# Kernel optimization log

Hardware: AMD Instinct MI355X
Metric: run time of the kernel (lower is better)

## Reference

```python
import jax, jax.numpy as jnp
import numpy as np

T, E, H, V, K = 1024, 300, 512, 100000, 12
START, STOP = 10, 11


def setup_inputs() -> dict:
    key = jax.random.key(0)
    ks = jax.random.split(key, 12)
    s = 0.05
    sentence = jax.random.randint(ks[0], (T,), 0, V, dtype=jnp.int32)
    tags = jax.random.randint(ks[1], (T,), 0, START, dtype=jnp.int32)  # real tags only
    word_embeds = jax.random.normal(ks[2], (V, E), jnp.float32) * 0.1

    def lstm_p(k):
        k1, k2 = jax.random.split(k)
        return (jax.random.normal(k1, (4 * H, E), jnp.float32) * s,
                jax.random.normal(k2, (4 * H, H), jnp.float32) * s,
                jnp.zeros(4 * H, jnp.float32), jnp.zeros(4 * H, jnp.float32))

    Wih_f, Whh_f, bih_f, bhh_f = lstm_p(ks[3])
    Wih_b, Whh_b, bih_b, bhh_b = lstm_p(ks[4])
    D = 2 * H
    attn_W = jax.random.normal(ks[5], (D, D), jnp.float32) * s
    attn_b = jnp.zeros(D, jnp.float32)
    h2h1_W = jax.random.normal(ks[6], (D, 2 * D), jnp.float32) * s
    h2h1_b = jnp.zeros(D, jnp.float32)
    tag_W = jax.random.normal(ks[7], (K, D), jnp.float32) * s
    tag_b = jnp.zeros(K, jnp.float32)
    transitions = jax.random.normal(ks[8], (K, K), jnp.float32) * 0.01
    transitions = transitions.at[START, :].set(-10000.0).at[:, STOP].set(-10000.0)
    return dict(sentence=sentence, tags=tags, word_embeds=word_embeds,
                Wih_f=Wih_f, Whh_f=Whh_f, bih_f=bih_f, bhh_f=bhh_f,
                Wih_b=Wih_b, Whh_b=Whh_b, bih_b=bih_b, bhh_b=bhh_b,
                attn_W=attn_W, attn_b=attn_b, h2h1_W=h2h1_W, h2h1_b=h2h1_b,
                tag_W=tag_W, tag_b=tag_b, transitions=transitions)


def _lstm_pass(x, Wih, Whh, bih, bhh):
    # x: [T, E] -> hs: [T, H]   (PyTorch LSTM gate order i,f,g,o)
    xg = x @ Wih.T + bih  # [T, 4H] precomputed input contribution

    def step(carry, g_in):
        h, c = carry
        g = g_in + h @ Whh.T + bhh
        i, f, gg, o = jnp.split(g, 4)
        i = jax.nn.sigmoid(i); f = jax.nn.sigmoid(f)
        gg = jnp.tanh(gg); o = jax.nn.sigmoid(o)
        c = f * c + i * gg
        h = o * jnp.tanh(c)
        return (h, c), h

    init = (jnp.zeros(H, x.dtype), jnp.zeros(H, x.dtype))
    _, hs = jax.lax.scan(step, init, xg)
    return hs


def reference(sentence, tags, word_embeds, Wih_f, Whh_f, bih_f, bhh_f,
              Wih_b, Whh_b, bih_b, bhh_b, attn_W, attn_b,
              h2h1_W, h2h1_b, tag_W, tag_b, transitions):
    x = word_embeds[sentence]                       # [T, E]  (dropout is eval no-op)
    h_fwd = _lstm_pass(x, Wih_f, Whh_f, bih_f, bhh_f)
    h_bwd = _lstm_pass(x[::-1], Wih_b, Whh_b, bih_b, bhh_b)[::-1]
    enc = jnp.concatenate([h_fwd, h_bwd], axis=-1)  # [T, 2H]

    # Attn 'general': energy(t, i) = enc[t] . (W enc[i] + b); vectorized per-timestep loop
    proj = enc @ attn_W.T + attn_b                  # [T, 2H]
    scores = enc @ proj.T                           # [T, T]
    w = jax.nn.softmax(scores, axis=-1)
    ctx = w @ enc                                   # [T, 2H]

    h1 = jnp.tanh(jnp.concatenate([enc, ctx], axis=-1) @ h2h1_W.T + h2h1_b)  # [T, 2H]
    feats = h1 @ tag_W.T + tag_b                    # [T, K]

    # CRF forward algorithm (log partition); transitions[to, from]
    alpha0 = jnp.full((K,), -10000.0, feats.dtype).at[START].set(0.0)

    def crf_step(alpha, feat):
        a = jax.nn.logsumexp(alpha[None, :] + transitions, axis=1) + feat
        return a, None

    alpha, _ = jax.lax.scan(crf_step, alpha0, feats)
    logZ = jax.nn.logsumexp(alpha + transitions[STOP])

    # gold path score (_score_sentence)
    pad_start = jnp.concatenate([jnp.array([START], tags.dtype), tags])
    pad_stop = jnp.concatenate([tags, jnp.array([STOP], tags.dtype)])
    gold = transitions[pad_stop, pad_start].sum() + feats[jnp.arange(T), tags].sum()

    return logZ - gold  # CRF negative log-likelihood for this sentence
```

## Files before the change

kernel.cpp:

```cpp
#include <hip/hip_runtime.h>
#include <hip/hip_fp16.h>

#define T_LEN 1024
#define E_DIM 300
#define H_DIM 512
#define D_DIM 1024
#define K_TAGS 12
#define G4 2048

typedef __attribute__((ext_vector_type(8))) short short8x;
typedef __attribute__((ext_vector_type(4))) float f32x4;

static __device__ __forceinline__ float frcp(float x){ return __builtin_amdgcn_rcpf(x); }
static __device__ __forceinline__ float sigm(float x){ return frcp(1.f + __expf(-x)); }
static __device__ __forceinline__ float ftanh(float x){
  const float e = __expf(2.f * fabsf(x));
  const float t = 1.f - 2.f * frcp(e + 1.f);
  return copysignf(t, x);
}
static __device__ __forceinline__ unsigned short f2b(float f){
  unsigned u = __float_as_uint(f);
  return (unsigned short)((u + 0x7fffu + ((u >> 16) & 1u)) >> 16);
}
static __device__ __forceinline__ uint4 pack8(const float* s){
  uint4 o;
  o.x = (unsigned)f2b(s[0]) | ((unsigned)f2b(s[1]) << 16);
  o.y = (unsigned)f2b(s[2]) | ((unsigned)f2b(s[3]) << 16);
  o.z = (unsigned)f2b(s[4]) | ((unsigned)f2b(s[5]) << 16);
  o.w = (unsigned)f2b(s[6]) | ((unsigned)f2b(s[7]) << 16);
  return o;
}

__global__ void k_gather(const int* __restrict__ sent, const float* __restrict__ we,
                         float* __restrict__ x){
  int idx = blockIdx.x*256 + threadIdx.x;
  if (idx < T_LEN*E_DIM){
    int t = idx / E_DIM, e = idx - t*E_DIM;
    x[idx] = we[(size_t)sent[t]*E_DIM + e];
  }
}

__global__ void k_init(unsigned* __restrict__ hbuf){
  int i = blockIdx.x*256 + threadIdx.x;
  if (i < 2048) hbuf[i] = 0u;
}

__global__ __launch_bounds__(256) void k_gemm_mfma(
    const float* __restrict__ Af, int lda, int arev,
    const float* __restrict__ Bf, const unsigned short* __restrict__ Bh, int ldb,
    const float* __restrict__ bias, int act,
    float* __restrict__ C, int ldc, int M, int N, int K)
{
  __shared__ __align__(16) unsigned short As[64*40];
  __shared__ __align__(16) unsigned short Bs[64*40];
  const int tid = threadIdx.x;
  const int bm = blockIdx.y*64, bn = blockIdx.x*64;
  const int r  = tid >> 2, c8 = (tid & 3) * 8;
  const int wave = tid >> 6, lane = tid & 63;
  const int wm = (wave >> 1) * 32, wn = (wave & 1) * 32;
  const int col = lane & 15, quad = lane >> 4;

  const int am = arev ? (M-1-(bm+r)) : (bm+r);
  const float* arow = Af + (size_t)am*lda;
  const float* brow = Bf ? (Bf + (size_t)(bn+r)*ldb) : (const float*)0;
  const unsigned short* brh = Bh ? (Bh + (size_t)(bn+r)*ldb) : (const unsigned short*)0;

  uint4* aw = (uint4*)(As + r*40 + c8);
  uint4* bw = (uint4*)(Bs + r*40 + c8);

  f32x4 acc[2][2];
  #pragma unroll
  for (int i=0;i<2;i++)
    #pragma unroll
    for (int j=0;j<2;j++) acc[i][j] = (f32x4){0.f,0.f,0.f,0.f};

  for (int k0 = 0; k0 < K; k0 += 32){
    uint4 avv, bvv;
    if (k0 + 32 <= K){
      avv = pack8(arow + k0 + c8);
      bvv = Bh ? *(const uint4*)(brh + k0 + c8) : pack8(brow + k0 + c8);
    } else {
      float ta[8], tb[8];
      #pragma unroll
      for (int i=0;i<8;i++){
        const int kk = k0 + c8 + i;
        ta[i] = (kk < K) ? arow[kk] : 0.f;
        tb[i] = (kk < K && Bf) ? brow[kk] : 0.f;
      }
      avv = pack8(ta); bvv = pack8(tb);
    }
    if (k0) __syncthreads();
    *aw = avv; *bw = bvv;
    __syncthreads();
    const short8x a0 = *(const short8x*)(As + (wm+col)*40    + quad*8);
    const short8x a1 = *(const short8x*)(As + (wm+16+col)*40 + quad*8);
    const short8x b0 = *(const short8x*)(Bs + (wn+col)*40    + quad*8);
    const short8x b1 = *(const short8x*)(Bs + (wn+16+col)*40 + quad*8);
    acc[0][0] = __builtin_amdgcn_mfma_f32_16x16x32_bf16(a0, b0, acc[0][0], 0, 0, 0);
    acc[0][1] = __builtin_amdgcn_mfma_f32_16x16x32_bf16(a0, b1, acc[0][1], 0, 0, 0);
    acc[1][0] = __builtin_amdgcn_mfma_f32_16x16x32_bf16(a1, b0, acc[1][0], 0, 0, 0);
    acc[1][1] = __builtin_amdgcn_mfma_f32_16x16x32_bf16(a1, b1, acc[1][1], 0, 0, 0);
  }

  #pragma unroll
  for (int mt=0;mt<2;mt++){
    #pragma unroll
    for (int nt=0;nt<2;nt++){
      const int cc = bn + wn + 16*nt + col;
      const float bs = bias ? bias[cc] : 0.f;
      #pragma unroll
      for (int i=0;i<4;i++){
        const int rr = bm + wm + 16*mt + quad*4 + i;
        float v = acc[mt][nt][i] + bs;
        if (act) v = ftanh(v);
        C[(size_t)rr*ldc + cc] = v;
      }
    }
  }
}

__global__ __launch_bounds__(256, 1) void k_lstm(
    const float* __restrict__ Whh_f, const float* __restrict__ Whh_b,
    const float* __restrict__ bih_f, const float* __restrict__ bhh_f,
    const float* __restrict__ bih_b, const float* __restrict__ bhh_b,
    const float* __restrict__ xg_f, const float* __restrict__ xg_b,
    unsigned* __restrict__ hbuf, float* __restrict__ enc)
{
  const int dir = blockIdx.x >> 5;
  const int w   = blockIdx.x & 31;
  const int tid = threadIdx.x;
  const int wave = tid >> 6, lane = tid & 63;
  const int col = lane & 15, quad = lane >> 4;

  const float* Whh = dir ? Whh_b : Whh_f;
  const float* xg  = dir ? xg_b  : xg_f;

  const int rowA = wave*H_DIM + w*16 + col;
  short8x w_frag[16];
  #pragma unroll
  for (int s=0;s<16;s++){
    const float* bp = Whh + (size_t)rowA*H_DIM + s*32 + quad*8;
    uint4 u = pack8(bp);
    w_frag[s] = *reinterpret_cast<short8x*>(&u);
  }

  float bias_r = 0.f, xg_cur = 0.f, c_reg = 0.f;
  int row2 = 0;
  if (tid < 64){
    row2 = (tid >> 4)*H_DIM + w*16 + (tid & 15);
    bias_r = dir ? (bih_b[row2] + bhh_b[row2]) : (bih_f[row2] + bhh_f[row2]);
    xg_cur = xg[row2];
  }

  __shared__ __align__(16) unsigned short lds_hb[512];
  __shared__ __align__(16) float raw[64];

  unsigned* hb = hbuf + dir*1024;

  for (int t = 1; t <= T_LEN; ++t){
    {
      unsigned* s0 = hb + ((t-1)&1)*512 + tid;
      const unsigned want = (unsigned)(t-1);
      unsigned v0 = __hip_atomic_load(s0,     __ATOMIC_RELAXED, __HIP_MEMORY_SCOPE_AGENT);
      unsigned v1 = __hip_atomic_load(s0+256, __ATOMIC_RELAXED, __HIP_MEMORY_SCOPE_AGENT);
      while (((v0 >> 16) != want) || ((v1 >> 16) != want)){
        v0 = __hip_atomic_load(s0,     __ATOMIC_RELAXED, __HIP_MEMORY_SCOPE_AGENT);
        v1 = __hip_atomic_load(s0+256, __ATOMIC_RELAXED, __HIP_MEMORY_SCOPE_AGENT);
      }
      lds_hb[tid]     = f2b(__half2float(__ushort_as_half((unsigned short)(v0 & 0xffffu))));
      lds_hb[tid+256] = f2b(__half2float(__ushort_as_half((unsigned short)(v1 & 0xffffu))));
    }
    __syncthreads();

    float xg_nxt = 0.f;
    if (tid < 64 && t < T_LEN) xg_nxt = xg[(size_t)t*G4 + row2];

    f32x4 a0 = (f32x4){0.f,0.f,0.f,0.f}, a1 = (f32x4){0.f,0.f,0.f,0.f};
    #pragma unroll
    for (int s=0;s<16;s+=2){
      const short8x b0 = *(const short8x*)(lds_hb + s*32     + quad*8);
      const short8x b1 = *(const short8x*)(lds_hb + (s+1)*32 + quad*8);
      a0 = __builtin_amdgcn_mfma_f32_16x16x32_bf16(w_frag[s],   b0, a0, 0, 0, 0);
      a1 = __builtin_amdgcn_mfma_f32_16x16x32_bf16(w_frag[s+1], b1, a1, 0, 0, 0);
    }
    if (col == 0){
      f32x4 asum = a0 + a1;
      *reinterpret_cast<f32x4*>(raw + wave*16 + quad*4) = asum;
    }
    __syncthreads();

    if (tid < 64){
      float v = raw[tid] + bias_r + xg_cur;
      const float va = ((tid >> 4) == 2) ? ftanh(v) : sigm(v);
      const int l2 = tid & 15;
      const float iv = __shfl(va, l2);
      const float fv = __shfl(va, l2 + 16);
      const float gg = __shfl(va, l2 + 32);
      const float ov = __shfl(va, l2 + 48);
      if (tid < 16){
        c_reg = fv*c_reg + iv*gg;
        const float hh = ov*ftanh(c_reg);
        const int hj = w*16 + tid;
        const unsigned hv = ((unsigned)t << 16) |
                            (unsigned)__half_as_ushort(__float2half(hh));
        __hip_atomic_store(hb + (t&1)*512 + hj, hv,
                           __ATOMIC_RELAXED, __HIP_MEMORY_SCOPE_AGENT);
        const int tt = dir ? (T_LEN - t) : (t - 1);
        enc[(size_t)tt*D_DIM + dir*H_DIM + hj] = hh;
      }
      xg_cur = xg_nxt;
    }
    __syncthreads();
  }
}

__global__ __launch_bounds__(256) void k_softmax(float* __restrict__ S){
  float* r = S + (size_t)blockIdx.x*1024;
  const int tid = threadIdx.x;
  float v[4];
  #pragma unroll
  for (int i=0;i<4;i++) v[i] = r[tid + i*256];
  float m = fmaxf(fmaxf(v[0],v[1]), fmaxf(v[2],v[3]));
  #pragma unroll
  for (int off=32; off>=1; off>>=1) m = fmaxf(m, __shfl_xor(m, off));
  __shared__ float red[4], red2[4];
  const int wid = tid >> 6, lane = tid & 63;
  if (lane == 0) red[wid] = m;
  __syncthreads();
  m = fmaxf(fmaxf(red[0],red[1]), fmaxf(red[2],red[3]));
  float s = 0.f;
  #pragma unroll
  for (int i=0;i<4;i++){ v[i] = __expf(v[i]-m); s += v[i]; }
  #pragma unroll
  for (int off=32; off>=1; off>>=1) s += __shfl_xor(s, off);
  if (lane == 0) red2[wid] = s;
  __syncthreads();
  s = red2[0]+red2[1]+red2[2]+red2[3];
  const float inv = frcp(s);
  #pragma unroll
  for (int i=0;i<4;i++) r[tid + i*256] = v[i]*inv;
}

__global__ void k_copy_enc(const float* __restrict__ enc, float* __restrict__ cat){
  int idx = blockIdx.x*256 + threadIdx.x;
  if (idx < T_LEN*D_DIM){
    int t = idx >> 10, d = idx & 1023;
    cat[(size_t)t*2048 + d] = enc[idx];
  }
}

__global__ __launch_bounds__(256) void k_castT(const float* __restrict__ src,
                                               unsigned short* __restrict__ dst){
  __shared__ float tile[32][33];
  const int bx = blockIdx.x*32, by = blockIdx.y*32;
  const int tx = threadIdx.x & 31, ty8 = threadIdx.x >> 5;
  #pragma unroll
  for (int i=ty8;i<32;i+=8) tile[i][tx] = src[(size_t)(by+i)*1024 + bx+tx];
  __syncthreads();
  #pragma unroll
  for (int i=ty8;i<32;i+=8) dst[(size_t)(bx+i)*1024 + by+tx] = f2b(tile[tx][i]);
}

__global__ __launch_bounds__(256) void k_feats(
    const float* __restrict__ h1, const float* __restrict__ tagW,
    const float* __restrict__ tagb, float* __restrict__ feats)
{
  const int t = blockIdx.x;
  const int wave = threadIdx.x >> 6, lane = threadIdx.x & 63;
  const float* hr = h1 + (size_t)t*D_DIM;
  float hv[16];
  #pragma unroll
  for (int i=0;i<16;i++) hv[i] = hr[lane + 64*i];
  #pragma unroll
  for (int j=0;j<3;j++){
    const int tag = wave*3 + j;
    const float* wr = tagW + (size_t)tag*D_DIM;
    float s = 0.f;
    #pragma unroll
    for (int i=0;i<16;i++) s += hv[i]*wr[lane + 64*i];
    #pragma unroll
    for (int off=32; off>=1; off>>=1) s += __shfl_xor(s, off);
    if (lane == 0) feats[(size_t)t*K_TAGS + tag] = s + tagb[tag];
  }
}

__global__ void k_crf(const float* __restrict__ feats, const float* __restrict__ trans,
                      const int* __restrict__ tags, float* __restrict__ out){
  const int tid = threadIdx.x;
  float gold = 0.f;
  for (int i = tid; i <= T_LEN; i += 64){
    const int to = (i < T_LEN) ? tags[i]   : 11;
    const int fr = (i == 0)    ? 10        : tags[i-1];
    gold += trans[to*K_TAGS + fr];
    if (i < T_LEN) gold += feats[(size_t)i*K_TAGS + tags[i]];
  }
  #pragma unroll
  for (int off=32; off>=1; off>>=1) gold += __shfl_xor(gold, off);

  float Trow[K_TAGS];
  if (tid < K_TAGS){
    #pragma unroll
    for (int j=0;j<K_TAGS;j++) Trow[j] = trans[tid*K_TAGS + j];
  }
  float alpha = (tid == 10) ? 0.f : -10000.f;
  for (int t=0;t<T_LEN;++t){
    float av[K_TAGS];
    #pragma unroll
    for (int j=0;j<K_TAGS;j++) av[j] = __shfl(alpha, j);
    if (tid < K_TAGS){
      float vv[K_TAGS], m = -1e30f;
      #pragma unroll
      for (int j=0;j<K_TAGS;j++){ vv[j] = av[j] + Trow[j]; m = fmaxf(m, vv[j]); }
      float s = 0.f;
      #pragma unroll
      for (int j=0;j<K_TAGS;j++) s += __expf(vv[j]-m);
      alpha = m + __logf(s) + feats[(size_t)t*K_TAGS + tid];
    }
  }
  float v = (tid < K_TAGS) ? (alpha + trans[11*K_TAGS + tid]) : -1e30f;
  float m = v;
  #pragma unroll
  for (int off=32; off>=1; off>>=1) m = fmaxf(m, __shfl_xor(m, off));
  float e = (tid < K_TAGS) ? __expf(v - m) : 0.f;
  #pragma unroll
  for (int off=32; off>=1; off>>=1) e += __shfl_xor(e, off);
  if (tid == 0) out[0] = (m + __logf(e)) - gold;
}

extern "C" void kernel_launch(void* const* d_in, const int* in_sizes, int n_in,
                              void* d_out, int out_size, void* d_ws, size_t ws_size,
                              hipStream_t stream)
{
  const int*   sentence = (const int*)d_in[0];
  const int*   tags     = (const int*)d_in[1];
  const float* we       = (const float*)d_in[2];
  const float* Wih_f    = (const float*)d_in[3];
  const float* Whh_f    = (const float*)d_in[4];
  const float* bih_f    = (const float*)d_in[5];
  const float* bhh_f    = (const float*)d_in[6];
  const float* Wih_b    = (const float*)d_in[7];
  const float* Whh_b    = (const float*)d_in[8];
  const float* bih_b    = (const float*)d_in[9];
  const float* bhh_b    = (const float*)d_in[10];
  const float* attn_W   = (const float*)d_in[11];
  const float* attn_b   = (const float*)d_in[12];
  const float* h2h1_W   = (const float*)d_in[13];
  const float* h2h1_b   = (const float*)d_in[14];
  const float* tag_W    = (const float*)d_in[15];
  const float* tag_b    = (const float*)d_in[16];
  const float* trans    = (const float*)d_in[17];
  float* out = (float*)d_out;

  float* ws     = (float*)d_ws;
  float* cat    = ws;
  float* reg2   = cat  + 2097152;
  float* enc    = reg2 + 2097152;
  float* proj   = enc  + 1048576;
  float* feats  = proj + 1048576;
  unsigned* hbuf= (unsigned*)(feats + 12288);
  float* xg_f   = cat;
  float* xg_b   = reg2;
  float* scores = reg2;
  float* h1     = reg2 + 1048576;
  float* x      = proj;
  unsigned short* encT = (unsigned short*)proj;

  k_gather<<<dim3((T_LEN*E_DIM + 255)/256), dim3(256), 0, stream>>>(sentence, we, x);
  k_init<<<dim3(8), dim3(256), 0, stream>>>(hbuf);
  k_gemm_mfma<<<dim3(32,16), dim3(256), 0, stream>>>(x, E_DIM, 0,
      Wih_f, nullptr, E_DIM, nullptr, 0, xg_f, G4, T_LEN, G4, E_DIM);
  k_gemm_mfma<<<dim3(32,16), dim3(256), 0, stream>>>(x, E_DIM, 1,
      Wih_b, nullptr, E_DIM, nullptr, 0, xg_b, G4, T_LEN, G4, E_DIM);
  k_lstm<<<dim3(64), dim3(256), 0, stream>>>(Whh_f, Whh_b, bih_f, bhh_f,
      bih_b, bhh_b, xg_f, xg_b, hbuf, enc);
  k_gemm_mfma<<<dim3(16,16), dim3(256), 0, stream>>>(enc, D_DIM, 0,
      attn_W, nullptr, D_DIM, attn_b, 0, proj, D_DIM, T_LEN, D_DIM, D_DIM);
  k_gemm_mfma<<<dim3(16,16), dim3(256), 0, stream>>>(enc, D_DIM, 0,
      proj, nullptr, D_DIM, nullptr, 0, scores, T_LEN, T_LEN, T_LEN, D_DIM);
  k_softmax<<<dim3(1024), dim3(256), 0, stream>>>(scores);
  k_copy_enc<<<dim3(4096), dim3(256), 0, stream>>>(enc, cat);
  k_castT<<<dim3(32,32), dim3(256), 0, stream>>>(enc, encT);
  k_gemm_mfma<<<dim3(16,16), dim3(256), 0, stream>>>(scores, T_LEN, 0,
      nullptr, encT, D_DIM, nullptr, 0, cat + 1024, 2048, T_LEN, D_DIM, T_LEN);
  k_gemm_mfma<<<dim3(16,16), dim3(256), 0, stream>>>(cat, 2048, 0,
      h2h1_W, nullptr, 2048, h2h1_b, 1, h1, D_DIM, T_LEN, D_DIM, 2048);
  k_feats<<<dim3(1024), dim3(256), 0, stream>>>(h1, tag_W, tag_b, feats);
  k_crf<<<dim3(1), dim3(64), 0, stream>>>(feats, trans, tags, out);
}
```

Measured before the change: 2.107 ms.

## Restructure LSTM recurrence into single-wave blocks polling hidden state directly

The persistent LSTM kernel changes from 64 blocks of 4 waves to 256 single-wave blocks, each owning 4 hidden units across all four gates. Each wave loads the tagged previous hidden state straight from global memory with cache-bypassing inline-asm loads into MFMA operands, removing the LDS staging and all __syncthreads. Hidden values are now stored as bf16 rather than fp16 converted to bf16. The CRF kernel also stages feats into shared memory in blocks, which shortens the serial per-step load latency. In exchange each wave spins over 32 chunks of global loads every step and more blocks take part in the cross-block handshake.

```diff
diff --git a/kernel.cpp b/kernel.cpp
--- a/kernel.cpp
+++ b/kernel.cpp
@@ -119,98 +119,119 @@
   }
 }
 
-__global__ __launch_bounds__(256, 1) void k_lstm(
+#define CHUNK_LIST(M) \
+  M(0,"0","16")      M(1,"128","144")   M(2,"256","272")   M(3,"384","400")   \
+  M(4,"512","528")   M(5,"640","656")   M(6,"768","784")   M(7,"896","912")   \
+  M(8,"1024","1040") M(9,"1152","1168") M(10,"1280","1296")M(11,"1408","1424")\
+  M(12,"1536","1552")M(13,"1664","1680")M(14,"1792","1808")M(15,"1920","1936")
+
+#define ISSUE_CHUNK(s,O0,O1) \
+  asm volatile("global_load_dwordx4 %0, %[p], off offset:" O0 " sc0 sc1\n\t" \
+               "global_load_dwordx4 %1, %[p], off offset:" O1 " sc0 sc1" \
+               : "=&v"(cl[s]), "=&v"(ch[s]) : [p] "v"(ap) : "memory");
+
+#define RETRY_CHUNK(s,O0,O1) if (mask & (1u<<s)) { ISSUE_CHUNK(s,O0,O1) }
+
+#define CHECK_CHUNK(s,O0,O1) \
+  if (!__all(chunk_ok(cl[s], ch[s], tagw))) mask |= (1u<<s);
+
+#define RECHECK_CHUNK(s,O0,O1) \
+  if ((mask & (1u<<s)) && !__all(chunk_ok(cl[s], ch[s], tagw))) nm |= (1u<<s);
+
+#define DECODE_MFMA(s,O0,O1) { \
+  uint4 pk; \
+  pk.x = __builtin_amdgcn_perm(cl[s].y, cl[s].x, 0x05040100u); \
+  pk.y = __builtin_amdgcn_perm(cl[s].w, cl[s].z, 0x05040100u); \
+  pk.z = __builtin_amdgcn_perm(ch[s].y, ch[s].x, 0x05040100u); \
+  pk.w = __builtin_amdgcn_perm(ch[s].w, ch[s].z, 0x05040100u); \
+  short8x bb = *reinterpret_cast<short8x*>(&pk); \
+  if (s & 1) a1 = __builtin_amdgcn_mfma_f32_16x16x32_bf16(w_frag[s], bb, a1, 0,0,0); \
+  else       a0 = __builtin_amdgcn_mfma_f32_16x16x32_bf16(w_frag[s], bb, a0, 0,0,0); }
+
+static __device__ __forceinline__ bool chunk_ok(uint4 a, uint4 b, unsigned tagw){
+  unsigned d = (a.x^tagw)|(a.y^tagw)|(a.z^tagw)|(a.w^tagw)
+             | (b.x^tagw)|(b.y^tagw)|(b.z^tagw)|(b.w^tagw);
+  return (d & 0xFFFF0000u) == 0u;
+}
+
+__global__ __launch_bounds__(64, 1) void k_lstm(
     const float* __restrict__ Whh_f, const float* __restrict__ Whh_b,
     const float* __restrict__ bih_f, const float* __restrict__ bhh_f,
     const float* __restrict__ bih_b, const float* __restrict__ bhh_b,
     const float* __restrict__ xg_f, const float* __restrict__ xg_b,
     unsigned* __restrict__ hbuf, float* __restrict__ enc)
 {
-  const int dir = blockIdx.x >> 5;
-  const int w   = blockIdx.x & 31;
-  const int tid = threadIdx.x;
-  const int wave = tid >> 6, lane = tid & 63;
+  const int dir = blockIdx.x >> 7;
+  const int wid = blockIdx.x & 127;
+  const int base_u = wid*4;
+  const int lane = threadIdx.x & 63;
   const int col = lane & 15, quad = lane >> 4;
+  const int u = lane & 3;
 
   const float* Whh = dir ? Whh_b : Whh_f;
   const float* xg  = dir ? xg_b  : xg_f;
 
-  const int rowA = wave*H_DIM + w*16 + col;
+  const int rowW = (col>>2)*H_DIM + base_u + (col&3);
+  const float* wr = Whh + (size_t)rowW*H_DIM;
   short8x w_frag[16];
   #pragma unroll
   for (int s=0;s<16;s++){
-    const float* bp = Whh + (size_t)rowA*H_DIM + s*32 + quad*8;
-    uint4 u = pack8(bp);
-    w_frag[s] = *reinterpret_cast<short8x*>(&u);
-  }
-
-  float bias_r = 0.f, xg_cur = 0.f, c_reg = 0.f;
-  int row2 = 0;
-  if (tid < 64){
-    row2 = (tid >> 4)*H_DIM + w*16 + (tid & 15);
-    bias_r = dir ? (bih_b[row2] + bhh_b[row2]) : (bih_f[row2] + bhh_f[row2]);
-    xg_cur = xg[row2];
-  }
-
-  __shared__ __align__(16) unsigned short lds_hb[512];
-  __shared__ __align__(16) float raw[64];
+    uint4 uu = pack8(wr + s*32 + quad*8);
+    w_frag[s] = *reinterpret_cast<short8x*>(&uu);
+  }
+
+  const int row2 = quad*H_DIM + base_u + u;
+  const float bias_r = dir ? (bih_b[row2] + bhh_b[row2]) : (bih_f[row2] + bhh_f[row2]);
+  float xg_cur = xg[row2];
+  float c_reg = 0.f;
 
   unsigned* hb = hbuf + dir*1024;
+  const unsigned* ap0 = hb + 0*512 + quad*8;
+  const unsigned* ap1 = hb + 1*512 + quad*8;
 
   for (int t = 1; t <= T_LEN; ++t){
-    {
-      unsigned* s0 = hb + ((t-1)&1)*512 + tid;
-      const unsigned want = (unsigned)(t-1);
-      unsigned v0 = __hip_atomic_load(s0,     __ATOMIC_RELAXED, __HIP_MEMORY_SCOPE_AGENT);
-      unsigned v1 = __hip_atomic_load(s0+256, __ATOMIC_RELAXED, __HIP_MEMORY_SCOPE_AGENT);
-      while (((v0 >> 16) != want) || ((v1 >> 16) != want)){
-        v0 = __hip_atomic_load(s0,     __ATOMIC_RELAXED, __HIP_MEMORY_SCOPE_AGENT);
-        v1 = __hip_atomic_load(s0+256, __ATOMIC_RELAXED, __HIP_MEMORY_SCOPE_AGENT);
-      }
-      lds_hb[tid]     = f2b(__half2float(__ushort_as_half((unsigned short)(v0 & 0xffffu))));
-      lds_hb[tid+256] = f2b(__half2float(__ushort_as_half((unsigned short)(v1 & 0xffffu))));
+    float xg_nxt = 0.f;
+    if (t < T_LEN) xg_nxt = xg[(size_t)t*G4 + row2];
+
+    const unsigned* ap = ((t-1)&1) ? ap1 : ap0;
+    const unsigned tagw = ((unsigned)(t-1)) << 16;
+    uint4 cl[16], ch[16];
+
+    CHUNK_LIST(ISSUE_CHUNK)
+    asm volatile("s_waitcnt vmcnt(0)" ::: "memory");
+
+    unsigned mask = 0u;
+    CHUNK_LIST(CHECK_CHUNK)
+    while (mask){
+      CHUNK_LIST(RETRY_CHUNK)
+      asm volatile("s_waitcnt vmcnt(0)" ::: "memory");
+      unsigned nm = 0u;
+      CHUNK_LIST(RECHECK_CHUNK)
+      mask = nm;
     }
-    __syncthreads();
-
-    float xg_nxt = 0.f;
-    if (tid < 64 && t < T_LEN) xg_nxt = xg[(size_t)t*G4 + row2];
 
     f32x4 a0 = (f32x4){0.f,0.f,0.f,0.f}, a1 = (f32x4){0.f,0.f,0.f,0.f};
-    #pragma unroll
-    for (int s=0;s<16;s+=2){
-      const short8x b0 = *(const short8x*)(lds_hb + s*32     + quad*8);
-      const short8x b1 = *(const short8x*)(lds_hb + (s+1)*32 + quad*8);
-      a0 = __builtin_amdgcn_mfma_f32_16x16x32_bf16(w_frag[s],   b0, a0, 0, 0, 0);
-      a1 = __builtin_amdgcn_mfma_f32_16x16x32_bf16(w_frag[s+1], b1, a1, 0, 0, 0);
+    CHUNK_LIST(DECODE_MFMA)
+    const f32x4 asum = a0 + a1;
+
+    const float au  = (u==0)?asum[0]:((u==1)?asum[1]:((u==2)?asum[2]:asum[3]));
+    const float val = au + bias_r + xg_cur;
+    const float act = (quad==2) ? ftanh(val) : sigm(val);
+    const float iv = __shfl(act, u);
+    const float fv = __shfl(act, u+16);
+    const float gg = __shfl(act, u+32);
+    const float ov = __shfl(act, u+48);
+    c_reg = fv*c_reg + iv*gg;
+    const float hh = ov*ftanh(c_reg);
+
+    if (lane < 4){
+      const unsigned pw = ((unsigned)t << 16) | (unsigned)f2b(hh);
+      __hip_atomic_store(hb + (t&1)*512 + base_u + lane, pw,
+                         __ATOMIC_RELAXED, __HIP_MEMORY_SCOPE_AGENT);
+      const int tt = dir ? (T_LEN - t) : (t - 1);
+      enc[(size_t)tt*D_DIM + dir*H_DIM + base_u + lane] = hh;
     }
-    if (col == 0){
-      f32x4 asum = a0 + a1;
-      *reinterpret_cast<f32x4*>(raw + wave*16 + quad*4) = asum;
-    }
-    __syncthreads();
-
-    if (tid < 64){
-      float v = raw[tid] + bias_r + xg_cur;
-      const float va = ((tid >> 4) == 2) ? ftanh(v) : sigm(v);
-      const int l2 = tid & 15;
-      const float iv = __shfl(va, l2);
-      const float fv = __shfl(va, l2 + 16);
-      const float gg = __shfl(va, l2 + 32);
-      const float ov = __shfl(va, l2 + 48);
-      if (tid < 16){
-        c_reg = fv*c_reg + iv*gg;
-        const float hh = ov*ftanh(c_reg);
-        const int hj = w*16 + tid;
-        const unsigned hv = ((unsigned)t << 16) |
-                            (unsigned)__half_as_ushort(__float2half(hh));
-        __hip_atomic_store(hb + (t&1)*512 + hj, hv,
-                           __ATOMIC_RELAXED, __HIP_MEMORY_SCOPE_AGENT);
-        const int tt = dir ? (T_LEN - t) : (t - 1);
-        enc[(size_t)tt*D_DIM + dir*H_DIM + hj] = hh;
-      }
-      xg_cur = xg_nxt;
-    }
-    __syncthreads();
+    xg_cur = xg_nxt;
   }
 }
 
@@ -287,6 +308,7 @@
 __global__ void k_crf(const float* __restrict__ feats, const float* __restrict__ trans,
                       const int* __restrict__ tags, float* __restrict__ out){
   const int tid = threadIdx.x;
+  __shared__ float fs[768];
   float gold = 0.f;
   for (int i = tid; i <= T_LEN; i += 64){
     const int to = (i < T_LEN) ? tags[i]   : 11;
@@ -303,19 +325,25 @@
     for (int j=0;j<K_TAGS;j++) Trow[j] = trans[tid*K_TAGS + j];
   }
   float alpha = (tid == 10) ? 0.f : -10000.f;
-  for (int t=0;t<T_LEN;++t){
-    float av[K_TAGS];
-    #pragma unroll
-    for (int j=0;j<K_TAGS;j++) av[j] = __shfl(alpha, j);
-    if (tid < K_TAGS){
-      float vv[K_TAGS], m = -1e30f;
+  for (int b=0;b<16;++b){
+    #pragma unroll
+    for (int r=0;r<12;r++) fs[tid + 64*r] = feats[b*768 + tid + 64*r];
+    __syncthreads();
+    for (int k=0;k<64;++k){
+      float av[K_TAGS];
       #pragma unroll
-      for (int j=0;j<K_TAGS;j++){ vv[j] = av[j] + Trow[j]; m = fmaxf(m, vv[j]); }
-      float s = 0.f;
-      #pragma unroll
-      for (int j=0;j<K_TAGS;j++) s += __expf(vv[j]-m);
-      alpha = m + __logf(s) + feats[(size_t)t*K_TAGS + tid];
+      for (int j=0;j<K_TAGS;j++) av[j] = __shfl(alpha, j);
+      if (tid < K_TAGS){
+        float vv[K_TAGS], m = -1e30f;
+        #pragma unroll
+        for (int j=0;j<K_TAGS;j++){ vv[j] = av[j] + Trow[j]; m = fmaxf(m, vv[j]); }
+        float s = 0.f;
+        #pragma unroll
+        for (int j=0;j<K_TAGS;j++) s += __expf(vv[j]-m);
+        alpha = m + __logf(s) + fs[k*K_TAGS + tid];
+      }
     }
+    __syncthreads();
   }
   float v = (tid < K_TAGS) ? (alpha + trans[11*K_TAGS + tid]) : -1e30f;
   float m = v;
@@ -371,7 +399,7 @@
       Wih_f, nullptr, E_DIM, nullptr, 0, xg_f, G4, T_LEN, G4, E_DIM);
   k_gemm_mfma<<<dim3(32,16), dim3(256), 0, stream>>>(x, E_DIM, 1,
       Wih_b, nullptr, E_DIM, nullptr, 0, xg_b, G4, T_LEN, G4, E_DIM);
-  k_lstm<<<dim3(64), dim3(256), 0, stream>>>(Whh_f, Whh_b, bih_f, bhh_f,
+  k_lstm<<<dim3(256), dim3(64), 0, stream>>>(Whh_f, Whh_b, bih_f, bhh_f,
       bih_b, bhh_b, xg_f, xg_b, hbuf, enc);
   k_gemm_mfma<<<dim3(16,16), dim3(256), 0, stream>>>(enc, D_DIM, 0,
       attn_W, nullptr, D_DIM, attn_b, 0, proj, D_DIM, T_LEN, D_DIM, D_DIM);
```

After: 3.819 ms. 1.81x slower.
